# Kernel optimization log

Hardware: AMD Instinct MI355X
Metric: run time of the kernel (lower is better)

The kernel has to match this reference:

```python
import jax, jax.numpy as jnp
import numpy as np

N_ROWS = 32768
CHANNELS = 4096

def setup_inputs() -> dict:
    key = jax.random.key(0)
    k1, k2 = jax.random.split(key)
    x = jax.random.normal(k1, (N_ROWS, CHANNELS), dtype=jnp.float32)
    # nn.Parameter(torch.ones(channels)); use uniform in (0.5, 1.5) around init for a nontrivial test
    diagonal = jax.random.uniform(k2, (CHANNELS,), dtype=jnp.float32, minval=0.5, maxval=1.5)
    return {"x": x, "diagonal": diagonal}

def reference(x, diagonal):
    # torch.matmul(x, torch.diag_embed(diagonal)) == x * diagonal (broadcast over last axis)
    return x * diagonal
```

## Files before the change

kernel.cpp:

```cpp
#include <hip/hip_runtime.h>


#define CH4 1024

typedef float f32x4 __attribute__((ext_vector_type(4)));

__global__ __launch_bounds__(1024)
void DiagonalLinear_wide(const f32x4* __restrict__ x,
                         const f32x4* __restrict__ diag,
                         f32x4* __restrict__ out,
                         unsigned int chunk) {
    const unsigned int tid = threadIdx.x;
    const f32x4 dv = diag[tid];
    unsigned int idx = blockIdx.x * chunk + tid;
    const unsigned int end = blockIdx.x * chunk + chunk;
#pragma unroll 4
    for (; idx < end; idx += 1024) {
        f32x4 v = __builtin_nontemporal_load(&x[idx]);
        __builtin_nontemporal_store(v * dv, &out[idx]);
    }
}

__global__ __launch_bounds__(256)
void DiagonalLinear_chunked(const f32x4* __restrict__ x,
                            const f32x4* __restrict__ diag,
                            f32x4* __restrict__ out,
                            unsigned int chunk) {
    const unsigned int tid  = threadIdx.x;
    const unsigned int iters = chunk >> 8;
    const f32x4 d0 = diag[tid];
    const f32x4 d1 = diag[tid + 256];
    const f32x4 d2 = diag[tid + 512];
    const f32x4 d3 = diag[tid + 768];
    unsigned int idx = blockIdx.x * chunk + tid;
    for (unsigned int k = 0; k < iters; k += 4, idx += 1024) {
        f32x4 a = __builtin_nontemporal_load(&x[idx]);
        __builtin_nontemporal_store(a * d0, &out[idx]);
        f32x4 b = __builtin_nontemporal_load(&x[idx + 256]);
        __builtin_nontemporal_store(b * d1, &out[idx + 256]);
        f32x4 c = __builtin_nontemporal_load(&x[idx + 512]);
        __builtin_nontemporal_store(c * d2, &out[idx + 512]);
        f32x4 d = __builtin_nontemporal_load(&x[idx + 768]);
        __builtin_nontemporal_store(d * d3, &out[idx + 768]);
    }
}

template <bool HOIST>
__global__ __launch_bounds__(256)
void DiagonalLinear_gs(const f32x4* __restrict__ x,
                       const f32x4* __restrict__ diag,
                       f32x4* __restrict__ out,
                       unsigned int n4) {
    const unsigned int stride = gridDim.x * blockDim.x;
    unsigned int i = blockIdx.x * blockDim.x + threadIdx.x;
    f32x4 dv;
    if (HOIST) dv = diag[i & (CH4 - 1)];
    for (; i < n4; i += stride) {
        f32x4 xv = __builtin_nontemporal_load(&x[i]);
        f32x4 dvv = HOIST ? dv : diag[i & (CH4 - 1)];
        __builtin_nontemporal_store(xv * dvv, &out[i]);
    }
}

extern "C" void kernel_launch(void* const* d_in, const int* in_sizes, int n_in,
                              void* d_out, int out_size, void* d_ws, size_t ws_size,
                              hipStream_t stream) {
    const float* x    = (const float*)d_in[0];
    const float* diag = (const float*)d_in[1];
    float* out        = (float*)d_out;

    const long long n  = (long long)in_sizes[0];
    const unsigned int n4 = (unsigned int)(n / 4);

    {
        const int grid = 512;
        const unsigned int chunk = n4 / grid;
        if ((long long)grid * chunk == (long long)n4 && (chunk & (CH4 - 1)) == 0) {
            DiagonalLinear_wide<<<grid, 1024, 0, stream>>>(
                (const f32x4*)x, (const f32x4*)diag, (f32x4*)out, chunk);
            return;
        }
    }
    {
        const int grid = 2048;
        const unsigned int chunk = n4 / grid;
        if ((long long)grid * chunk == (long long)n4 &&
            (chunk & (CH4 - 1)) == 0 && ((chunk >> 8) & 3) == 0) {
            DiagonalLinear_chunked<<<grid, 256, 0, stream>>>(
                (const f32x4*)x, (const f32x4*)diag, (f32x4*)out, chunk);
            return;
        }
    }
    const int block = 256;
    long long want = ((long long)n4 + block - 1) / block;
    int g = (int)(want < 2048 ? want : 2048);
    const unsigned int stride = (unsigned int)g * block;
    if ((stride & (CH4 - 1)) == 0) {
        DiagonalLinear_gs<true><<<g, block, 0, stream>>>(
            (const f32x4*)x, (const f32x4*)diag, (f32x4*)out, n4);
    } else {
        DiagonalLinear_gs<false><<<g, block, 0, stream>>>(
            (const f32x4*)x, (const f32x4*)diag, (f32x4*)out, n4);
    }
}
```

Measured before the change: 192.6 us.

## Assign contiguous per-wavefront chunks instead of block-strided chunks

Adds a kernel where each 64-lane wavefront streams its own contiguous slice of the array, so each wave walks a sequential address range rather than interleaving with the other waves of its block. The diagonal vector is reloaded each iteration through cached loads, since a wave's slice spans many channel positions. It also removes the unused 256-thread chunked kernel path. The change aims at better DRAM page locality, at the cost of an extra diag load per iteration and less coalescing across waves.

```diff
diff --git a/kernel.cpp b/kernel.cpp
--- a/kernel.cpp
+++ b/kernel.cpp
@@ -4,6 +4,22 @@
 #define CH4 1024
 
 typedef float f32x4 __attribute__((ext_vector_type(4)));
+
+__global__ __launch_bounds__(1024)
+void DiagonalLinear_wavechunk(const f32x4* __restrict__ x,
+                              const f32x4* __restrict__ diag,
+                              f32x4* __restrict__ out,
+                              unsigned int wchunk) {
+    const unsigned int lane  = threadIdx.x & 63u;
+    const unsigned int gwave = (blockIdx.x * blockDim.x + threadIdx.x) >> 6;
+    unsigned int idx = gwave * wchunk + lane;
+    const unsigned int end = gwave * wchunk + wchunk;
+    for (; idx < end; idx += 64) {
+        f32x4 v  = __builtin_nontemporal_load(&x[idx]);
+        f32x4 dv = diag[idx & (CH4 - 1)];
+        __builtin_nontemporal_store(v * dv, &out[idx]);
+    }
+}
 
 __global__ __launch_bounds__(1024)
 void DiagonalLinear_wide(const f32x4* __restrict__ x,
@@ -18,30 +34,6 @@
     for (; idx < end; idx += 1024) {
         f32x4 v = __builtin_nontemporal_load(&x[idx]);
         __builtin_nontemporal_store(v * dv, &out[idx]);
-    }
-}
-
-__global__ __launch_bounds__(256)
-void DiagonalLinear_chunked(const f32x4* __restrict__ x,
-                            const f32x4* __restrict__ diag,
-                            f32x4* __restrict__ out,
-                            unsigned int chunk) {
-    const unsigned int tid  = threadIdx.x;
-    const unsigned int iters = chunk >> 8;
-    const f32x4 d0 = diag[tid];
-    const f32x4 d1 = diag[tid + 256];
-    const f32x4 d2 = diag[tid + 512];
-    const f32x4 d3 = diag[tid + 768];
-    unsigned int idx = blockIdx.x * chunk + tid;
-    for (unsigned int k = 0; k < iters; k += 4, idx += 1024) {
-        f32x4 a = __builtin_nontemporal_load(&x[idx]);
-        __builtin_nontemporal_store(a * d0, &out[idx]);
-        f32x4 b = __builtin_nontemporal_load(&x[idx + 256]);
-        __builtin_nontemporal_store(b * d1, &out[idx + 256]);
-        f32x4 c = __builtin_nontemporal_load(&x[idx + 512]);
-        __builtin_nontemporal_store(c * d2, &out[idx + 512]);
-        f32x4 d = __builtin_nontemporal_load(&x[idx + 768]);
-        __builtin_nontemporal_store(d * d3, &out[idx + 768]);
     }
 }
 
@@ -73,20 +65,20 @@
     const unsigned int n4 = (unsigned int)(n / 4);
 
     {
+        const int grid = 512, block = 1024;
+        const unsigned int nwaves = (unsigned int)grid * block / 64;
+        const unsigned int wchunk = n4 / nwaves;
+        if ((long long)nwaves * wchunk == (long long)n4 && (wchunk & 63u) == 0) {
+            DiagonalLinear_wavechunk<<<grid, block, 0, stream>>>(
+                (const f32x4*)x, (const f32x4*)diag, (f32x4*)out, wchunk);
+            return;
+        }
+    }
+    {
         const int grid = 512;
         const unsigned int chunk = n4 / grid;
         if ((long long)grid * chunk == (long long)n4 && (chunk & (CH4 - 1)) == 0) {
             DiagonalLinear_wide<<<grid, 1024, 0, stream>>>(
-                (const f32x4*)x, (const f32x4*)diag, (f32x4*)out, chunk);
-            return;
-        }
-    }
-    {
-        const int grid = 2048;
-        const unsigned int chunk = n4 / grid;
-        if ((long long)grid * chunk == (long long)n4 &&
-            (chunk & (CH4 - 1)) == 0 && ((chunk >> 8) & 3) == 0) {
-            DiagonalLinear_chunked<<<grid, 256, 0, stream>>>(
                 (const f32x4*)x, (const f32x4*)diag, (f32x4*)out, chunk);
             return;
         }
```

Result: slower. 217.5 us (+12.9%).
